# Optimization experiments

Hardware: AMD Instinct MI355X
Metric: run time of the kernel (lower is better)

## Reference

```python
import jax, jax.numpy as jnp
import numpy as np


def setup_inputs() -> dict:
    key = jax.random.key(0)
    k1, k2, k3 = jax.random.split(key, 3)
    bs, seqlen, hidden = 2, 2048, 1024
    s, h = 4, 256  # sqrt_n_heads, head_size
    std = 0.02
    num_layers = 12
    hidden_states = jax.random.normal(k1, (bs, seqlen, hidden), dtype=jnp.float32)
    q_scale = 1.0 / np.sqrt(2.0 * num_layers * h)
    queries = jax.random.normal(k2, (s, h, h * s), dtype=jnp.float32) * std * q_scale
    combiners = jax.random.normal(k3, (s, h * s, h), dtype=jnp.float32) * (std * q_scale)
    return {"hidden_states": hidden_states, "queries": queries, "combiners": combiners}


def reference(hidden_states, queries, combiners):
    # queries: [s1, h, s*h], combiners: [s1, s*h, h]
    s, h, _ = queries.shape
    bs, S, E = hidden_states.shape
    x = hidden_states.reshape(bs, S, s, h)            # [b, t, s, h]
    qw = queries.reshape(s, h, s, h)                  # [s1, h_in, s2, h_out]
    # projected queries, already permuted to [s2, b, t, s1, f]
    Q = jnp.einsum('btae,aeqf->qbtaf', x, qw)
    # pre-attention scores: [s2, b, t, s1, u] (u = key position)  ~O(S^2)
    pre = jnp.einsum('qbtaf,buqf->qbtau', Q, x)
    # attention output, permuted to [s1, b, t, s2, g]
    attn = jnp.einsum('qbtau,buqg->abtqg', pre, x)
    attn = attn.reshape(s, bs, S, s * h)              # [s1, b, t, s2*h]
    out = jnp.einsum('abtk,akg->btag', attn, combiners)
    return out.reshape(bs, S, s * h)
```

## Files before the change

kernel.cpp:

```cpp
#include <hip/hip_runtime.h>
#include <hip/hip_bf16.h>


typedef unsigned short u16;
using short8  = __attribute__((ext_vector_type(8))) short;
using floatx4 = __attribute__((ext_vector_type(4))) float;

__device__ inline u16 f2bf(float f) {
    unsigned u = __float_as_uint(f);
    unsigned r = u + 0x7fffu + ((u >> 16) & 1u);
    return (u16)(r >> 16);
}

template <typename T>
__device__ inline void stage64(const T* __restrict__ src, long ld,
                               u16* __restrict__ dst, int tid) {
#pragma unroll
    for (int it = 0; it < 4; ++it) {
        const int flat = (it * 256 + tid) * 4;
        const int kl = flat & 63, rl = flat >> 6;
        ushort4 v;
        if (sizeof(T) == 4) {
            const float4 f = *(const float4*)&((const float*)src)[(long)rl * ld + kl];
            v.x = f2bf(f.x); v.y = f2bf(f.y); v.z = f2bf(f.z); v.w = f2bf(f.w);
        } else {
            v = *(const ushort4*)&((const u16*)src)[(long)rl * ld + kl];
        }
        const int chunk = ((kl >> 5) * 4 + (rl >> 4)) * 64 + ((kl >> 3) & 3) * 16 + (rl & 15);
        *(ushort4*)&dst[chunk * 8 + (kl & 7)] = v;
    }
}

__device__ inline void stage_km64(const float* __restrict__ src, long ld,
                                  u16* __restrict__ dst, int tid) {
#pragma unroll
    for (int it = 0; it < 4; ++it) {
        const int flat = (it * 256 + tid) * 4;
        const int m = flat & 63, k = flat >> 6;
        const float4 f = *(const float4*)&src[(long)k * ld + m];
        const int cb_ = ((k >> 5) * 4 + (m >> 4)) * 64 + ((k & 31) >> 3) * 16 + (m & 15);
        const int j = k & 7;
        dst[(cb_ + 0) * 8 + j] = f2bf(f.x);
        dst[(cb_ + 1) * 8 + j] = f2bf(f.y);
        dst[(cb_ + 2) * 8 + j] = f2bf(f.z);
        dst[(cb_ + 3) * 8 + j] = f2bf(f.w);
    }
}

template <typename TA, typename TB, bool AKM, bool BKM, bool ATOMIC>
__device__ inline void gemm_tile(const TA* __restrict__ A, long lda,
                                 const TB* __restrict__ B, long ldb,
                                 float* __restrict__ C, long ldc,
                                 int K, int m0, int n0) {
    __shared__ u16 As[4096];
    __shared__ u16 Bs[4096];
    const int tid = threadIdx.x, lane = tid & 63, w = tid >> 6;
    const int IA = (w & 1) * 2, JB = (w >> 1) * 2;
    floatx4 acc[2][2] = {};

    for (int k0 = 0; k0 < K; k0 += 64) {
        if (AKM) stage_km64((const float*)A + (long)k0 * lda, lda, As, tid);
        else     stage64(A + k0, lda, As, tid);
        if (BKM) stage_km64((const float*)B + (long)k0 * ldb, ldb, Bs, tid);
        else     stage64(B + k0, ldb, Bs, tid);
        __syncthreads();
#pragma unroll
        for (int s = 0; s < 2; ++s) {
            short8 af[2], bfr[2];
#pragma unroll
            for (int i = 0; i < 2; ++i)
                af[i] = *(const short8*)&As[((s * 4 + IA + i) * 64 + lane) * 8];
#pragma unroll
            for (int j = 0; j < 2; ++j)
                bfr[j] = *(const short8*)&Bs[((s * 4 + JB + j) * 64 + lane) * 8];
#pragma unroll
            for (int i = 0; i < 2; ++i)
#pragma unroll
                for (int j = 0; j < 2; ++j)
                    acc[i][j] = __builtin_amdgcn_mfma_f32_16x16x32_bf16(af[i], bfr[j], acc[i][j], 0, 0, 0);
        }
        __syncthreads();
    }
    const int rb = (lane >> 4) * 4, col = lane & 15;
#pragma unroll
    for (int i = 0; i < 2; ++i)
#pragma unroll
        for (int j = 0; j < 2; ++j)
#pragma unroll
            for (int r = 0; r < 4; ++r) {
                const int gm = m0 + (IA + i) * 16 + rb + r;
                const int gn = n0 + (JB + j) * 16 + col;
                float* p = &C[(long)gm * ldc + gn];
                if (ATOMIC) atomicAdd(p, acc[i][j][r]); else *p = acc[i][j][r];
            }
}

__global__ __launch_bounds__(256) void k_gram(const float* __restrict__ x,
                                              float* __restrict__ G) {
    const int tile = blockIdx.x, bq = blockIdx.y, split = blockIdx.z;
    const int tm = tile >> 2, tn = tile & 3;
    const int b = bq >> 2, q = bq & 3;
    const float* base = x + (long)b * 2097152 + (long)split * 256 * 1024 + q * 256;
    gemm_tile<float, float, true, true, true>(
        base + tm * 64, 1024,
        base + tn * 64, 1024,
        G + (long)bq * 65536, 256,
        256, tm * 64, tn * 64);
}

__global__ __launch_bounds__(256) void k_2a(const float* __restrict__ comb,
                                            const float* __restrict__ G,
                                            float* __restrict__ Tt) {
    const int tile = blockIdx.x, i = blockIdx.y;
    const int tm = tile >> 2, tn = tile & 3;
    const int q = i & 3, ba = i >> 2, b = ba >> 2, a = ba & 3;
    gemm_tile<float, float, true, false, false>(
        comb + (long)a * 262144 + (long)q * 256 * 256 + tm * 64, 256,
        G + (long)(b * 4 + q) * 65536 + (long)tn * 64 * 256, 256,
        Tt + (long)ba * 262144, 1024,
        256, tm * 64, q * 256 + tn * 64);
}

__global__ __launch_bounds__(256) void k_2b(const float* __restrict__ Tt,
                                            const float* __restrict__ qw,
                                            float* __restrict__ Wt) {
    const int tile = blockIdx.x, ba = blockIdx.y, split = blockIdx.z;
    const int tm = tile >> 2, tn = tile & 3;
    const int a = ba & 3;
    gemm_tile<float, float, false, false, true>(
        Tt + (long)ba * 262144 + (long)tm * 64 * 1024 + split * 256, 1024,
        qw + (long)a * 262144 + (long)tn * 64 * 1024 + split * 256, 1024,
        Wt + (long)ba * 65536, 256,
        256, tm * 64, tn * 64);
}

__global__ __launch_bounds__(256) void k_3(const float* __restrict__ x,
                                           const float* __restrict__ Wt,
                                           float* __restrict__ out) {
    const int tl = blockIdx.x, ba = blockIdx.y;
    const int tm = tl >> 2, tn = tl & 3;
    const int b = ba >> 2, a = ba & 3;
    gemm_tile<float, float, false, false, false>(
        x + (long)b * 2097152 + (long)tm * 64 * 1024 + a * 256, 1024,
        Wt + (long)ba * 65536 + (long)tn * 64 * 256, 256,
        out + (long)b * 2097152 + a * 256, 1024,
        256, tm * 64, tn * 64);
}

extern "C" void kernel_launch(void* const* d_in, const int* in_sizes, int n_in,
                              void* d_out, int out_size, void* d_ws, size_t ws_size,
                              hipStream_t stream) {
    const float* x    = (const float*)d_in[0];
    const float* qw   = (const float*)d_in[1];
    const float* comb = (const float*)d_in[2];
    float* out = (float*)d_out;

    char* ws = (char*)d_ws;
    float* G  = (float*)(ws);
    float* Wt = (float*)(ws + (2u << 20));
    float* Tt = (float*)(ws + (4u << 20));

    hipMemsetAsync(d_ws, 0, 4u << 20, stream);
    k_gram<<<dim3(16, 8, 8), 256, 0, stream>>>(x, G);
    k_2a  <<<dim3(16, 32),   256, 0, stream>>>(comb, G, Tt);
    k_2b  <<<dim3(16, 8, 4), 256, 0, stream>>>(Tt, qw, Wt);
    k_3   <<<dim3(128, 8),   256, 0, stream>>>(x, Wt, out);
}
```

Before: 147.7 us.

## Replace atomic split-K Gram with two partial buffers summed in consumer

The Gram kernel now uses 2 K-splits of 1024 instead of 8 splits of 256. Each split writes its own partial buffer with plain stores instead of atomicAdd. The next GEMM sums the two partials while staging its B operand. Zeroing of Wt moves into the Gram kernel, so the separate memset launch is dropped. The cost is fewer blocks (256 instead of 1024) with longer K loops, which lowers parallelism, plus an extra partial read in k_2a.

```diff
diff --git a/kernel.cpp b/kernel.cpp
--- a/kernel.cpp
+++ b/kernel.cpp
@@ -31,6 +31,23 @@
     }
 }
 
+__device__ inline void stage64_sum2(const float* __restrict__ s0,
+                                    const float* __restrict__ s1, long ld,
+                                    u16* __restrict__ dst, int tid) {
+#pragma unroll
+    for (int it = 0; it < 4; ++it) {
+        const int flat = (it * 256 + tid) * 4;
+        const int kl = flat & 63, rl = flat >> 6;
+        const float4 f = *(const float4*)&s0[(long)rl * ld + kl];
+        const float4 g = *(const float4*)&s1[(long)rl * ld + kl];
+        ushort4 v;
+        v.x = f2bf(f.x + g.x); v.y = f2bf(f.y + g.y);
+        v.z = f2bf(f.z + g.z); v.w = f2bf(f.w + g.w);
+        const int chunk = ((kl >> 5) * 4 + (rl >> 4)) * 64 + ((kl >> 3) & 3) * 16 + (rl & 15);
+        *(ushort4*)&dst[chunk * 8 + (kl & 7)] = v;
+    }
+}
+
 __device__ inline void stage_km64(const float* __restrict__ src, long ld,
                                   u16* __restrict__ dst, int tid) {
 #pragma unroll
@@ -47,9 +64,10 @@
     }
 }
 
-template <typename TA, typename TB, bool AKM, bool BKM, bool ATOMIC>
+template <typename TA, typename TB, bool AKM, bool BKM, bool BSUM2, bool ATOMIC>
 __device__ inline void gemm_tile(const TA* __restrict__ A, long lda,
                                  const TB* __restrict__ B, long ldb,
+                                 long partStride,
                                  float* __restrict__ C, long ldc,
                                  int K, int m0, int n0) {
     __shared__ u16 As[4096];
@@ -61,7 +79,9 @@
     for (int k0 = 0; k0 < K; k0 += 64) {
         if (AKM) stage_km64((const float*)A + (long)k0 * lda, lda, As, tid);
         else     stage64(A + k0, lda, As, tid);
-        if (BKM) stage_km64((const float*)B + (long)k0 * ldb, ldb, Bs, tid);
+        if (BSUM2) stage64_sum2((const float*)B + k0,
+                                (const float*)B + partStride + k0, ldb, Bs, tid);
+        else if (BKM) stage_km64((const float*)B + (long)k0 * ldb, ldb, Bs, tid);
         else     stage64(B + k0, ldb, Bs, tid);
         __syncthreads();
 #pragma unroll
@@ -96,27 +116,35 @@
 }
 
 __global__ __launch_bounds__(256) void k_gram(const float* __restrict__ x,
-                                              float* __restrict__ G) {
+                                              float* __restrict__ Gp,
+                                              float* __restrict__ Wt) {
     const int tile = blockIdx.x, bq = blockIdx.y, split = blockIdx.z;
     const int tm = tile >> 2, tn = tile & 3;
     const int b = bq >> 2, q = bq & 3;
-    const float* base = x + (long)b * 2097152 + (long)split * 256 * 1024 + q * 256;
-    gemm_tile<float, float, true, true, true>(
+    {
+        const int bl = tile + 16 * bq + 128 * split;
+        float4 zero = {0.f, 0.f, 0.f, 0.f};
+        float4* wz = (float4*)Wt + (long)bl * 512 + threadIdx.x * 2;
+        wz[0] = zero; wz[1] = zero;
+    }
+    const float* base = x + (long)b * 2097152 + (long)split * 1024 * 1024 + q * 256;
+    gemm_tile<float, float, true, true, false, false>(
         base + tm * 64, 1024,
-        base + tn * 64, 1024,
-        G + (long)bq * 65536, 256,
-        256, tm * 64, tn * 64);
+        base + tn * 64, 1024, 0,
+        Gp + (long)(split * 8 + bq) * 65536, 256,
+        1024, tm * 64, tn * 64);
 }
 
 __global__ __launch_bounds__(256) void k_2a(const float* __restrict__ comb,
-                                            const float* __restrict__ G,
+                                            const float* __restrict__ Gp,
                                             float* __restrict__ Tt) {
     const int tile = blockIdx.x, i = blockIdx.y;
     const int tm = tile >> 2, tn = tile & 3;
     const int q = i & 3, ba = i >> 2, b = ba >> 2, a = ba & 3;
-    gemm_tile<float, float, true, false, false>(
+    gemm_tile<float, float, true, false, true, false>(
         comb + (long)a * 262144 + (long)q * 256 * 256 + tm * 64, 256,
-        G + (long)(b * 4 + q) * 65536 + (long)tn * 64 * 256, 256,
+        Gp + (long)(b * 4 + q) * 65536 + (long)tn * 64 * 256, 256,
+        (long)8 * 65536,
         Tt + (long)ba * 262144, 1024,
         256, tm * 64, q * 256 + tn * 64);
 }
@@ -127,9 +155,9 @@
     const int tile = blockIdx.x, ba = blockIdx.y, split = blockIdx.z;
     const int tm = tile >> 2, tn = tile & 3;
     const int a = ba & 3;
-    gemm_tile<float, float, false, false, true>(
+    gemm_tile<float, float, false, false, false, true>(
         Tt + (long)ba * 262144 + (long)tm * 64 * 1024 + split * 256, 1024,
-        qw + (long)a * 262144 + (long)tn * 64 * 1024 + split * 256, 1024,
+        qw + (long)a * 262144 + (long)tn * 64 * 1024 + split * 256, 1024, 0,
         Wt + (long)ba * 65536, 256,
         256, tm * 64, tn * 64);
 }
@@ -140,9 +168,9 @@
     const int tl = blockIdx.x, ba = blockIdx.y;
     const int tm = tl >> 2, tn = tl & 3;
     const int b = ba >> 2, a = ba & 3;
-    gemm_tile<float, float, false, false, false>(
+    gemm_tile<float, float, false, false, false, false>(
         x + (long)b * 2097152 + (long)tm * 64 * 1024 + a * 256, 1024,
-        Wt + (long)ba * 65536 + (long)tn * 64 * 256, 256,
+        Wt + (long)ba * 65536 + (long)tn * 64 * 256, 256, 0,
         out + (long)b * 2097152 + a * 256, 1024,
         256, tm * 64, tn * 64);
 }
@@ -156,13 +184,12 @@
     float* out = (float*)d_out;
 
     char* ws = (char*)d_ws;
-    float* G  = (float*)(ws);
-    float* Wt = (float*)(ws + (2u << 20));
-    float* Tt = (float*)(ws + (4u << 20));
+    float* Gp = (float*)(ws);
+    float* Wt = (float*)(ws + (4u << 20));
+    float* Tt = (float*)(ws + (6u << 20));
 
-    hipMemsetAsync(d_ws, 0, 4u << 20, stream);
-    k_gram<<<dim3(16, 8, 8), 256, 0, stream>>>(x, G);
-    k_2a  <<<dim3(16, 32),   256, 0, stream>>>(comb, G, Tt);
+    k_gram<<<dim3(16, 8, 2), 256, 0, stream>>>(x, Gp, Wt);
+    k_2a  <<<dim3(16, 32),   256, 0, stream>>>(comb, Gp, Tt);
     k_2b  <<<dim3(16, 8, 4), 256, 0, stream>>>(Tt, qw, Wt);
     k_3   <<<dim3(128, 8),   256, 0, stream>>>(x, Wt, out);
 }
```

Result: slower. 169.4 us (+14.7%).
